# Optimization experiments

Hardware: AMD Instinct MI355X
Metric: run time of the kernel (lower is better)

## Reference

```python
import jax, jax.numpy as jnp
import numpy as np

N_NODES = 16384
N_GRAPHS = 64
NODES_PER_GRAPH = N_NODES // N_GRAPHS
F_IN = 128
E_DIM = 256
N_HEADS = 8
MLP = 1024
N_LAYERS = 4
N_CLASSES = 10
N_EDGES = 262144
LN_EPS = 1e-5


def setup_inputs() -> dict:
    key = jax.random.key(0)
    ks = jax.random.split(key, 32)
    s = 0.02
    inp = {
        "x": jax.random.normal(ks[0], (N_NODES, F_IN), jnp.float32),
        "edge_idx": jax.random.randint(ks[1], (2, N_EDGES), 0, N_NODES, jnp.int32),
        "batch": (jnp.arange(N_NODES, dtype=jnp.int32) // NODES_PER_GRAPH),
        "pos_enc": jax.random.normal(ks[2], (N_NODES, E_DIM), jnp.float32),
        # GCNConv params (torch Linear convention: W is [out, in])
        "gcn_w": jax.random.normal(ks[3], (F_IN, F_IN), jnp.float32) * s,
        "gcn_b": jnp.zeros((F_IN,), jnp.float32),
        "cls": jax.random.normal(ks[4], (E_DIM,), jnp.float32),
        "emb_w": jax.random.normal(ks[5], (E_DIM, F_IN), jnp.float32) * s,
        "emb_b": jnp.zeros((E_DIM,), jnp.float32),
        # stacked transformer-encoder-layer params over L layers
        "in_w": jax.random.normal(ks[6], (N_LAYERS, 3 * E_DIM, E_DIM), jnp.float32) * s,
        "in_b": jnp.zeros((N_LAYERS, 3 * E_DIM), jnp.float32),
        "out_w": jax.random.normal(ks[7], (N_LAYERS, E_DIM, E_DIM), jnp.float32) * s,
        "out_b": jnp.zeros((N_LAYERS, E_DIM), jnp.float32),
        "lin1_w": jax.random.normal(ks[8], (N_LAYERS, MLP, E_DIM), jnp.float32) * s,
        "lin1_b": jnp.zeros((N_LAYERS, MLP), jnp.float32),
        "lin2_w": jax.random.normal(ks[9], (N_LAYERS, E_DIM, MLP), jnp.float32) * s,
        "lin2_b": jnp.zeros((N_LAYERS, E_DIM), jnp.float32),
        "ln1_g": jnp.ones((N_LAYERS, E_DIM), jnp.float32),
        "ln1_beta": jnp.zeros((N_LAYERS, E_DIM), jnp.float32),
        "ln2_g": jnp.ones((N_LAYERS, E_DIM), jnp.float32),
        "ln2_beta": jnp.zeros((N_LAYERS, E_DIM), jnp.float32),
        "fc_w": jax.random.normal(ks[10], (N_CLASSES, E_DIM), jnp.float32) * s,
        "fc_b": jnp.zeros((N_CLASSES,), jnp.float32),
    }
    return inp


def _layer_norm(h, g, b):
    mu = jnp.mean(h, axis=-1, keepdims=True)
    var = jnp.mean(jnp.square(h - mu), axis=-1, keepdims=True)
    return (h - mu) * jax.lax.rsqrt(var + LN_EPS) * g + b


def _gcn_conv(x, edge_idx, gcn_w, gcn_b):
    # PyG GCNConv: lin -> add self-loops -> sym-normalized scatter-add -> +bias
    xw = x @ gcn_w.T                                             # [N, F]
    ar = jnp.arange(N_NODES, dtype=edge_idx.dtype)
    ei = jnp.concatenate([edge_idx, jnp.stack([ar, ar])], axis=1)
    row, col = ei[0], ei[1]
    deg = jax.ops.segment_sum(jnp.ones(ei.shape[1], xw.dtype), col, num_segments=N_NODES)
    dinv = jax.lax.rsqrt(deg)                                    # deg >= 1 (self loops)
    norm = dinv[row] * dinv[col]                                 # [E+N]
    out = jax.ops.segment_sum(norm[:, None] * xw[row], col, num_segments=N_NODES)
    return out + gcn_b


def reference(x, edge_idx, batch, pos_enc, gcn_w, gcn_b, cls, emb_w, emb_b,
              in_w, in_b, out_w, out_b, lin1_w, lin1_b, lin2_w, lin2_b,
              ln1_g, ln1_beta, ln2_g, ln2_beta, fc_w, fc_b):
    h = _gcn_conv(x, edge_idx, gcn_w, gcn_b)
    h = jax.nn.relu(h)
    h = h @ emb_w.T + emb_b + pos_enc                            # [N, E_DIM]
    # batch = arange // NODES_PER_GRAPH (contiguous equal-size graphs):
    # per-graph loop == batched reshape
    h = h.reshape(N_GRAPHS, NODES_PER_GRAPH, E_DIM)
    cls_tok = jnp.broadcast_to(cls, (N_GRAPHS, 1, E_DIM))
    h = jnp.concatenate([cls_tok, h], axis=1)                    # [G, S, E]
    S = NODES_PER_GRAPH + 1
    dh = E_DIM // N_HEADS
    scale = 1.0 / jnp.sqrt(jnp.asarray(dh, h.dtype))
    for l in range(N_LAYERS):
        # post-LN TransformerEncoderLayer (torch default), dropout off
        qkv = jnp.einsum('gse,fe->gsf', h, in_w[l]) + in_b[l]    # [G, S, 3E]
        q, k, v = jnp.split(qkv, 3, axis=-1)
        q = q.reshape(N_GRAPHS, S, N_HEADS, dh).transpose(0, 2, 1, 3)
        k = k.reshape(N_GRAPHS, S, N_HEADS, dh).transpose(0, 2, 1, 3)
        v = v.reshape(N_GRAPHS, S, N_HEADS, dh).transpose(0, 2, 1, 3)
        att = jax.nn.softmax(jnp.einsum('ghqd,ghkd->ghqk', q, k) * scale, axis=-1)
        o = jnp.einsum('ghqk,ghkd->ghqd', att, v)
        o = o.transpose(0, 2, 1, 3).reshape(N_GRAPHS, S, E_DIM)
        o = jnp.einsum('gse,fe->gsf', o, out_w[l]) + out_b[l]
        h = _layer_norm(h + o, ln1_g[l], ln1_beta[l])
        f = jax.nn.relu(jnp.einsum('gse,me->gsm', h, lin1_w[l]) + lin1_b[l])
        f = jnp.einsum('gsm,em->gse', f, lin2_w[l]) + lin2_b[l]
        h = _layer_norm(h + f, ln2_g[l], ln2_beta[l])
    cls_out = h[:, 0, :]                                         # [G, E]
    return cls_out @ fc_w.T + fc_b                               # [G, C]
```

## Files before the change

### kernel.cpp

```cpp
#include <hip/hip_runtime.h>
#include <cstddef>

#define N_NODES 16384
#define N_GRAPHS 64
#define NPG 256
#define F_IN 128
#define E_DIM 256
#define N_HEADS 8
#define DH 32
#define MLP 1024
#define N_LAYERS 4
#define N_CLASSES 10
#define N_EDGES 262144
#define S_LEN 257
#define M_ROWS (N_GRAPHS * S_LEN)
#define M_PAD 16512
#define LN_EPS 1e-5f

typedef __attribute__((ext_vector_type(8))) short bf16x8;
typedef __attribute__((ext_vector_type(4))) float f32x4;

__device__ inline unsigned short f2b1(float f) {
    unsigned u = __float_as_uint(f);
    unsigned r = (u + 0x7fffu + ((u >> 16) & 1u)) >> 16;
    return (unsigned short)r;
}

#define GLOBAL_LOAD_LDS16(g, l) \
    __builtin_amdgcn_global_load_lds((__attribute__((address_space(1))) const void*)(g), \
                                     (__attribute__((address_space(3))) void*)(l), 16, 0, 0)

__global__ void f2b4(const float* __restrict__ in, unsigned short* __restrict__ out, int n4) {
    int i = blockIdx.x * 256 + threadIdx.x;
    if (i < n4) {
        float4 v = ((const float4*)in)[i];
        ushort4 o;
        o.x = f2b1(v.x); o.y = f2b1(v.y); o.z = f2b1(v.z); o.w = f2b1(v.w);
        ((ushort4*)out)[i] = o;
    }
}

__global__ __launch_bounds__(256) void gemm_mfma(
    const unsigned short* __restrict__ A, const unsigned short* __restrict__ W,
    const float* __restrict__ bias, const float* __restrict__ add,
    float* __restrict__ outF, unsigned short* __restrict__ outB,
    int M, int N, int K, int relu)
{
    __shared__ __align__(16) unsigned short As[128 * 32];
    __shared__ __align__(16) unsigned short Bs[128 * 32];
    const int tid = threadIdx.x;
    const int wave = tid >> 6;
    const int lane = tid & 63;
    const int bm = blockIdx.y * 128;
    const int bn = blockIdx.x * 128;

    const int srow = (lane >> 2);
    const int scol = (lane & 3) * 8;
    const size_t a_r0 = (size_t)(bm + wave * 16 + srow) * K + scol;
    const size_t b_r0 = (size_t)(bn + wave * 16 + srow) * K + scol;
    unsigned short* ldsA0 = &As[wave * 512];
    unsigned short* ldsA1 = &As[(wave + 4) * 512];
    unsigned short* ldsB0 = &Bs[wave * 512];
    unsigned short* ldsB1 = &Bs[(wave + 4) * 512];

    const int wm = (wave & 1) * 64;
    const int wn = (wave >> 1) * 64;
    const int fr = lane & 15;
    const int fk = (lane >> 4) * 8;

    f32x4 acc[4][4];
#pragma unroll
    for (int i = 0; i < 4; ++i)
#pragma unroll
        for (int j = 0; j < 4; ++j)
            acc[i][j] = (f32x4){0.f, 0.f, 0.f, 0.f};

    for (int k0 = 0; k0 < K; k0 += 32) {
        __syncthreads();
        GLOBAL_LOAD_LDS16(A + a_r0 + k0, ldsA0);
        GLOBAL_LOAD_LDS16(A + a_r0 + (size_t)64 * K + k0, ldsA1);
        GLOBAL_LOAD_LDS16(W + b_r0 + k0, ldsB0);
        GLOBAL_LOAD_LDS16(W + b_r0 + (size_t)64 * K + k0, ldsB1);
        __syncthreads();

        bf16x8 a[4], b[4];
#pragma unroll
        for (int i = 0; i < 4; ++i)
            a[i] = *(const bf16x8*)&As[(wm + i * 16 + fr) * 32 + fk];
#pragma unroll
        for (int j = 0; j < 4; ++j)
            b[j] = *(const bf16x8*)&Bs[(wn + j * 16 + fr) * 32 + fk];
#pragma unroll
        for (int i = 0; i < 4; ++i)
#pragma unroll
            for (int j = 0; j < 4; ++j)
                acc[i][j] = __builtin_amdgcn_mfma_f32_16x16x32_bf16(a[i], b[j], acc[i][j], 0, 0, 0);
    }

    const int er = (lane >> 4) * 4;
    const int ec = lane & 15;
#pragma unroll
    for (int j = 0; j < 4; ++j) {
        const int col = bn + wn + j * 16 + ec;
        const float bs = bias ? bias[col] : 0.f;
#pragma unroll
        for (int i = 0; i < 4; ++i) {
#pragma unroll
            for (int r = 0; r < 4; ++r) {
                const int row = bm + wm + i * 16 + er + r;
                float v = acc[i][j][r] + bs;
                if (add)  v += add[(size_t)row * N + col];
                if (relu) v = fmaxf(v, 0.f);
                if (outF) outF[(size_t)row * N + col] = v;
                if (outB) outB[(size_t)row * N + col] = f2b1(v);
            }
        }
    }
}

__global__ void deg_count(const int* __restrict__ ei, float* __restrict__ deg) {
    int e = blockIdx.x * blockDim.x + threadIdx.x;
    if (e < N_EDGES) atomicAdd(&deg[ei[N_EDGES + e]], 1.0f);
}

__global__ void make_dinv(float* __restrict__ deg) {
    int i = blockIdx.x * blockDim.x + threadIdx.x;
    if (i < N_NODES) deg[i] = rsqrtf(deg[i] + 1.0f);
}

__global__ void edge_agg(const float* __restrict__ xw, const float* __restrict__ dinv,
                         const int* __restrict__ ei, float* __restrict__ agg) {
    int e = blockIdx.x;
    int f = threadIdx.x;
    int r = ei[e];
    int c = ei[N_EDGES + e];
    float nrm = dinv[r] * dinv[c];
    atomicAdd(&agg[(size_t)c * F_IN + f], nrm * xw[(size_t)r * F_IN + f]);
}

__global__ void gcn_finish(const float* __restrict__ agg, const float* __restrict__ xw,
                           const float* __restrict__ dinv, const float* __restrict__ b,
                           unsigned short* __restrict__ aggb) {
    int i = blockIdx.x;
    int f = threadIdx.x;
    float di = dinv[i];
    size_t idx = (size_t)i * F_IN + f;
    float v = agg[idx] + di * di * xw[idx] + b[f];
    aggb[idx] = f2b1(fmaxf(v, 0.f));
}

__global__ void assemble_h(const float* __restrict__ emb, const float* __restrict__ cls,
                           float* __restrict__ h, unsigned short* __restrict__ hb) {
    int row = blockIdx.x;
    int f = threadIdx.x;
    int g = row / S_LEN, s = row % S_LEN;
    float v = (s == 0) ? cls[f] : emb[((size_t)g * NPG + (s - 1)) * E_DIM + f];
    h[(size_t)row * E_DIM + f] = v;
    hb[(size_t)row * E_DIM + f] = f2b1(v);
}

__global__ __launch_bounds__(256) void attn_mfma(const unsigned short* __restrict__ qkvb,
                                                 unsigned short* __restrict__ ob) {
    const int g  = blockIdx.x >> 3;
    const int hh = blockIdx.x & 7;
    __shared__ __align__(16) unsigned short Ks[272 * 32];
    __shared__ __align__(16) unsigned short VT[32 * 288];
    __shared__ __align__(16) unsigned short Ps[4 * 16 * 288];
    const int tid  = threadIdx.x;
    const int wave = tid >> 6;
    const int lane = tid & 63;
    const int quad = lane >> 4;
    const int l16  = lane & 15;
    const size_t grow0 = (size_t)g * S_LEN;

    for (int s = tid; s < 272; s += 256) {
        uint4* dst = (uint4*)&Ks[s * 32];
        if (s < S_LEN) {
            const uint4* src = (const uint4*)(qkvb + (grow0 + s) * 768 + 256 + hh * 32);
            dst[0] = src[0]; dst[1] = src[1]; dst[2] = src[2]; dst[3] = src[3];
        } else {
            uint4 z = {0u, 0u, 0u, 0u};
            dst[0] = z; dst[1] = z; dst[2] = z; dst[3] = z;
        }
    }
    for (int s = tid; s < 288; s += 256) {
        unsigned short t[32];
        if (s < S_LEN) {
            const uint4* src = (const uint4*)(qkvb + (grow0 + s) * 768 + 512 + hh * 32);
            ((uint4*)t)[0] = src[0]; ((uint4*)t)[1] = src[1];
            ((uint4*)t)[2] = src[2]; ((uint4*)t)[3] = src[3];
        } else {
#pragma unroll
            for (int d = 0; d < 32; ++d) t[d] = 0;
        }
#pragma unroll
        for (int d = 0; d < 32; ++d) VT[d * 288 + s] = t[d];
    }
    unsigned short* Pw = &Ps[wave * 16 * 288];
    for (int i = lane; i < 256; i += 64)
        Pw[(i >> 4) * 288 + 272 + (i & 15)] = 0;
    __syncthreads();

    const float scale = 0.17677669529663687f;
    for (int qt = wave; qt < 17; qt += 4) {
        const int qrow_l = qt * 16 + l16;
        bf16x8 aq = *(const bf16x8*)(qkvb + (grow0 + qrow_l) * 768 + hh * 32 + quad * 8);

        f32x4 sc[17];
#pragma unroll
        for (int kt = 0; kt < 17; ++kt) {
            bf16x8 bk = *(const bf16x8*)&Ks[(kt * 16 + l16) * 32 + quad * 8];
            f32x4 z = (f32x4){0.f, 0.f, 0.f, 0.f};
            sc[kt] = __builtin_amdgcn_mfma_f32_16x16x32_bf16(aq, bk, z, 0, 0, 0);
        }

        float lsum[4] = {0.f, 0.f, 0.f, 0.f};
#pragma unroll
        for (int kt = 0; kt < 17; ++kt) {
#pragma unroll
            for (int r = 0; r < 4; ++r) {
                float p = __expf(sc[kt][r] * scale);
                if (kt == 16 && l16 != 0) p = 0.f;
                lsum[r] += p;
                Pw[(quad * 4 + r) * 288 + kt * 16 + l16] = f2b1(p);
            }
        }
#pragma unroll
        for (int r = 0; r < 4; ++r) {
            float s = lsum[r];
            s += __shfl_xor(s, 1, 64);
            s += __shfl_xor(s, 2, 64);
            s += __shfl_xor(s, 4, 64);
            s += __shfl_xor(s, 8, 64);
            lsum[r] = s;
        }

        f32x4 o0 = (f32x4){0.f, 0.f, 0.f, 0.f};
        f32x4 o1 = (f32x4){0.f, 0.f, 0.f, 0.f};
#pragma unroll
        for (int c = 0; c < 9; ++c) {
            bf16x8 ap  = *(const bf16x8*)&Pw[l16 * 288 + c * 32 + quad * 8];
            bf16x8 bv0 = *(const bf16x8*)&VT[l16 * 288 + c * 32 + quad * 8];
            bf16x8 bv1 = *(const bf16x8*)&VT[(16 + l16) * 288 + c * 32 + quad * 8];
            o0 = __builtin_amdgcn_mfma_f32_16x16x32_bf16(ap, bv0, o0, 0, 0, 0);
            o1 = __builtin_amdgcn_mfma_f32_16x16x32_bf16(ap, bv1, o1, 0, 0, 0);
        }

#pragma unroll
        for (int r = 0; r < 4; ++r) {
            int row_l = qt * 16 + quad * 4 + r;
            if (row_l < S_LEN) {
                float inv = 1.f / lsum[r];
                size_t orow = (grow0 + row_l) * E_DIM + hh * 32;
                ob[orow + l16]      = f2b1(o0[r] * inv);
                ob[orow + 16 + l16] = f2b1(o1[r] * inv);
            }
        }
    }
}

__global__ __launch_bounds__(256) void ln_residual(float* __restrict__ h, const float* __restrict__ res,
                                                   const float* __restrict__ g, const float* __restrict__ b,
                                                   unsigned short* __restrict__ hb) {
    __shared__ float ws1[4], ws2[4];
    __shared__ float mu_s, rstd_s;
    const int row = blockIdx.x;
    const int t = threadIdx.x;
    size_t idx = (size_t)row * E_DIM + t;
    float v = h[idx] + res[idx];
    float s1 = v, s2 = v * v;
#pragma unroll
    for (int off = 32; off > 0; off >>= 1) {
        s1 += __shfl_down(s1, off, 64);
        s2 += __shfl_down(s2, off, 64);
    }
    int wid = t >> 6, lane = t & 63;
    if (lane == 0) { ws1[wid] = s1; ws2[wid] = s2; }
    __syncthreads();
    if (t == 0) {
        float a1 = ws1[0] + ws1[1] + ws1[2] + ws1[3];
        float a2 = ws2[0] + ws2[1] + ws2[2] + ws2[3];
        float mu = a1 * (1.f / 256.f);
        float var = a2 * (1.f / 256.f) - mu * mu;
        mu_s = mu;
        rstd_s = rsqrtf(var + LN_EPS);
    }
    __syncthreads();
    float o = (v - mu_s) * rstd_s * g[t] + b[t];
    h[idx] = o;
    hb[idx] = f2b1(o);
}

__global__ void fc_kernel(const float* __restrict__ h, const float* __restrict__ w,
                          const float* __restrict__ b, float* __restrict__ out) {
    int g = blockIdx.x;
    __shared__ float row[E_DIM];
    int t = threadIdx.x;
    row[t] = h[(size_t)g * S_LEN * E_DIM + t];
    __syncthreads();
    if (t < N_CLASSES) {
        float s = 0.f;
        for (int j = 0; j < E_DIM; ++j) s += row[j] * w[t * E_DIM + j];
        out[g * N_CLASSES + t] = s + b[t];
    }
}

extern "C" void kernel_launch(void* const* d_in, const int* in_sizes, int n_in,
                              void* d_out, int out_size, void* d_ws, size_t ws_size,
                              hipStream_t stream) {
    const float* x       = (const float*)d_in[0];
    const int*   edgei   = (const int*)  d_in[1];
    const float* pos_enc = (const float*)d_in[3];
    const float* gcn_w   = (const float*)d_in[4];
    const float* gcn_b   = (const float*)d_in[5];
    const float* cls     = (const float*)d_in[6];
    const float* emb_w   = (const float*)d_in[7];
    const float* emb_b   = (const float*)d_in[8];
    const float* in_w    = (const float*)d_in[9];
    const float* in_b    = (const float*)d_in[10];
    const float* out_w   = (const float*)d_in[11];
    const float* out_b   = (const float*)d_in[12];
    const float* lin1_w  = (const float*)d_in[13];
    const float* lin1_b  = (const float*)d_in[14];
    const float* lin2_w  = (const float*)d_in[15];
    const float* lin2_b  = (const float*)d_in[16];
    const float* ln1_g   = (const float*)d_in[17];
    const float* ln1_be  = (const float*)d_in[18];
    const float* ln2_g   = (const float*)d_in[19];
    const float* ln2_be  = (const float*)d_in[20];
    const float* fc_w    = (const float*)d_in[21];
    const float* fc_b    = (const float*)d_in[22];
    float* out = (float*)d_out;

    float* ws = (float*)d_ws;
    float* h    = ws;
    float* tmp  = h    + (size_t)M_PAD * E_DIM;
    float* qkv  = tmp  + (size_t)M_PAD * E_DIM;
    float* xw   = qkv  + (size_t)M_PAD * 768;
    float* agg  = xw   + (size_t)N_NODES * F_IN;
    float* deg  = agg  + (size_t)N_NODES * F_IN;
    unsigned short* ub     = (unsigned short*)(deg + N_NODES);
    unsigned short* hb     = ub;
    unsigned short* attnob = hb     + (size_t)M_PAD * E_DIM;
    unsigned short* fbufb  = attnob + (size_t)M_PAD * E_DIM;
    unsigned short* xb     = fbufb  + (size_t)M_PAD * MLP;
    unsigned short* aggb   = xb     + (size_t)N_NODES * F_IN;
    unsigned short* gcn_wb = aggb   + (size_t)N_NODES * F_IN;
    unsigned short* emb_wb = gcn_wb + (size_t)F_IN * F_IN;
    unsigned short* in_wb  = emb_wb + (size_t)E_DIM * F_IN;
    unsigned short* out_wb = in_wb  + (size_t)N_LAYERS * 768 * E_DIM;
    unsigned short* lin1_wb= out_wb + (size_t)N_LAYERS * E_DIM * E_DIM;
    unsigned short* lin2_wb= lin1_wb+ (size_t)N_LAYERS * MLP * E_DIM;
    float* emb_out = qkv;
    unsigned short* qkvb = (unsigned short*)qkv;

    f2b4<<<(N_NODES * F_IN / 4 + 255) / 256, 256, 0, stream>>>(x, xb, N_NODES * F_IN / 4);
    f2b4<<<(F_IN * F_IN / 4 + 255) / 256, 256, 0, stream>>>(gcn_w, gcn_wb, F_IN * F_IN / 4);
    f2b4<<<(E_DIM * F_IN / 4 + 255) / 256, 256, 0, stream>>>(emb_w, emb_wb, E_DIM * F_IN / 4);
    f2b4<<<(N_LAYERS * 768 * E_DIM / 4 + 255) / 256, 256, 0, stream>>>(in_w, in_wb, N_LAYERS * 768 * E_DIM / 4);
    f2b4<<<(N_LAYERS * E_DIM * E_DIM / 4 + 255) / 256, 256, 0, stream>>>(out_w, out_wb, N_LAYERS * E_DIM * E_DIM / 4);
    f2b4<<<(N_LAYERS * MLP * E_DIM / 4 + 255) / 256, 256, 0, stream>>>(lin1_w, lin1_wb, N_LAYERS * MLP * E_DIM / 4);
    f2b4<<<(N_LAYERS * E_DIM * MLP / 4 + 255) / 256, 256, 0, stream>>>(lin2_w, lin2_wb, N_LAYERS * E_DIM * MLP / 4);

    hipMemsetAsync(deg, 0, N_NODES * sizeof(float), stream);
    hipMemsetAsync(agg, 0, (size_t)N_NODES * F_IN * sizeof(float), stream);
    deg_count<<<(N_EDGES + 255) / 256, 256, 0, stream>>>(edgei, deg);
    make_dinv<<<(N_NODES + 255) / 256, 256, 0, stream>>>(deg);
    gemm_mfma<<<dim3(F_IN / 128, N_NODES / 128), 256, 0, stream>>>(
        xb, gcn_wb, nullptr, nullptr, xw, nullptr, N_NODES, F_IN, F_IN, 0);
    edge_agg<<<N_EDGES, F_IN, 0, stream>>>(xw, deg, edgei, agg);
    gcn_finish<<<N_NODES, F_IN, 0, stream>>>(agg, xw, deg, gcn_b, aggb);

    gemm_mfma<<<dim3(E_DIM / 128, N_NODES / 128), 256, 0, stream>>>(
        aggb, emb_wb, emb_b, pos_enc, emb_out, nullptr, N_NODES, E_DIM, F_IN, 0);
    assemble_h<<<M_ROWS, E_DIM, 0, stream>>>(emb_out, cls, h, hb);

    for (int l = 0; l < N_LAYERS; ++l) {
        gemm_mfma<<<dim3(768 / 128, M_PAD / 128), 256, 0, stream>>>(
            hb, in_wb + (size_t)l * 768 * E_DIM, in_b + (size_t)l * 768, nullptr,
            nullptr, qkvb, M_PAD, 768, E_DIM, 0);
        attn_mfma<<<N_GRAPHS * N_HEADS, 256, 0, stream>>>(qkvb, attnob);
        gemm_mfma<<<dim3(E_DIM / 128, M_PAD / 128), 256, 0, stream>>>(
            attnob, out_wb + (size_t)l * E_DIM * E_DIM, out_b + (size_t)l * E_DIM, nullptr,
            tmp, nullptr, M_PAD, E_DIM, E_DIM, 0);
        ln_residual<<<M_ROWS, E_DIM, 0, stream>>>(h, tmp, ln1_g + l * E_DIM, ln1_be + l * E_DIM, hb);
        gemm_mfma<<<dim3(MLP / 128, M_PAD / 128), 256, 0, stream>>>(
            hb, lin1_wb + (size_t)l * MLP * E_DIM, lin1_b + (size_t)l * MLP, nullptr,
            nullptr, fbufb, M_PAD, MLP, E_DIM, 1);
        gemm_mfma<<<dim3(E_DIM / 128, M_PAD / 128), 256, 0, stream>>>(
            fbufb, lin2_wb + (size_t)l * E_DIM * MLP, lin2_b + (size_t)l * E_DIM, nullptr,
            tmp, nullptr, M_PAD, E_DIM, MLP, 0);
        ln_residual<<<M_ROWS, E_DIM, 0, stream>>>(h, tmp, ln2_g + l * E_DIM, ln2_be + l * E_DIM, hb);
    }

    fc_kernel<<<N_GRAPHS, E_DIM, 0, stream>>>(h, fc_w, fc_b, out);
}
```

Before: 944.7 us.

## Fuse LayerNorm into projection GEMMs, CSR-gather GCN aggregation, batch weight casts

Replaces the out-projection and MLP-down GEMMs plus separate residual LayerNorm kernels with a single full-row GEMM that applies bias, residual and LayerNorm in its epilogue, removing the fp32 temp round trip. GCN aggregation is rebuilt as a CSR layout (degree scan plus edge scatter) followed by a per-node gather, replacing per-feature float atomics. The seven bf16 cast launches are merged into one grid-stride kernel. Risks include lower GEMM parallelism in the 64-row fused tiles, a single-block scan, and nondeterministic edge order within CSR rows.

```diff
diff --git a/kernel.cpp b/kernel.cpp
--- a/kernel.cpp
+++ b/kernel.cpp
@@ -30,13 +30,23 @@
     __builtin_amdgcn_global_load_lds((__attribute__((address_space(1))) const void*)(g), \
                                      (__attribute__((address_space(3))) void*)(l), 16, 0, 0)
 
-__global__ void f2b4(const float* __restrict__ in, unsigned short* __restrict__ out, int n4) {
-    int i = blockIdx.x * 256 + threadIdx.x;
-    if (i < n4) {
-        float4 v = ((const float4*)in)[i];
-        ushort4 o;
-        o.x = f2b1(v.x); o.y = f2b1(v.y); o.z = f2b1(v.z); o.w = f2b1(v.w);
-        ((ushort4*)out)[i] = o;
+struct F2BJobs {
+    const float* src[7];
+    unsigned short* dst[7];
+    int n4[7];
+};
+__global__ __launch_bounds__(256) void f2b_all(F2BJobs jobs) {
+#pragma unroll 1
+    for (int r = 0; r < 7; ++r) {
+        const float4* s = (const float4*)jobs.src[r];
+        ushort4* d = (ushort4*)jobs.dst[r];
+        const int n4 = jobs.n4[r];
+        for (int i = blockIdx.x * 256 + threadIdx.x; i < n4; i += gridDim.x * 256) {
+            float4 v = s[i];
+            ushort4 o;
+            o.x = f2b1(v.x); o.y = f2b1(v.y); o.z = f2b1(v.z); o.w = f2b1(v.w);
+            d[i] = o;
+        }
     }
 }
 
@@ -118,35 +128,153 @@
     }
 }
 
+__global__ __launch_bounds__(256) void gemm_ln(
+    const unsigned short* __restrict__ A, const unsigned short* __restrict__ W,
+    const float* __restrict__ bias, const float* __restrict__ g,
+    const float* __restrict__ beta,
+    float* __restrict__ h, unsigned short* __restrict__ hb, int K)
+{
+    __shared__ __align__(16) unsigned short As[64 * 32];
+    __shared__ __align__(16) unsigned short Bs[256 * 32];
+    const int tid  = threadIdx.x;
+    const int wave = tid >> 6;
+    const int lane = tid & 63;
+    const int quad = lane >> 4;
+    const int l16  = lane & 15;
+    const int bm   = blockIdx.x * 64;
+
+    const int srow = lane >> 2;
+    const int scol = (lane & 3) * 8;
+    const size_t a_r0 = (size_t)(bm + wave * 16 + srow) * K + scol;
+    unsigned short* ldsA = &As[wave * 512];
+
+    f32x4 acc[16];
+#pragma unroll
+    for (int j = 0; j < 16; ++j) acc[j] = (f32x4){0.f, 0.f, 0.f, 0.f};
+
+    for (int k0 = 0; k0 < K; k0 += 32) {
+        __syncthreads();
+        GLOBAL_LOAD_LDS16(A + a_r0 + k0, ldsA);
+#pragma unroll
+        for (int cc = 0; cc < 4; ++cc) {
+            const int c = wave + cc * 4;
+            GLOBAL_LOAD_LDS16(W + (size_t)(c * 16 + srow) * K + scol + k0, &Bs[c * 512]);
+        }
+        __syncthreads();
+        bf16x8 a = *(const bf16x8*)&As[(wave * 16 + l16) * 32 + quad * 8];
+#pragma unroll
+        for (int j = 0; j < 16; ++j) {
+            bf16x8 b = *(const bf16x8*)&Bs[(j * 16 + l16) * 32 + quad * 8];
+            acc[j] = __builtin_amdgcn_mfma_f32_16x16x32_bf16(a, b, acc[j], 0, 0, 0);
+        }
+    }
+
+    const int row0 = bm + wave * 16 + quad * 4;
+    float gv[16], bv[16], biasv[16];
+#pragma unroll
+    for (int j = 0; j < 16; ++j) {
+        const int col = j * 16 + l16;
+        gv[j] = g[col]; bv[j] = beta[col]; biasv[j] = bias[col];
+    }
+#pragma unroll
+    for (int r = 0; r < 4; ++r) {
+        const int row = row0 + r;
+        float v[16];
+        float s1 = 0.f, s2 = 0.f;
+#pragma unroll
+        for (int j = 0; j < 16; ++j) {
+            const int col = j * 16 + l16;
+            float t = acc[j][r] + biasv[j] + h[(size_t)row * E_DIM + col];
+            v[j] = t; s1 += t; s2 += t * t;
+        }
+        s1 += __shfl_xor(s1, 1, 64); s2 += __shfl_xor(s2, 1, 64);
+        s1 += __shfl_xor(s1, 2, 64); s2 += __shfl_xor(s2, 2, 64);
+        s1 += __shfl_xor(s1, 4, 64); s2 += __shfl_xor(s2, 4, 64);
+        s1 += __shfl_xor(s1, 8, 64); s2 += __shfl_xor(s2, 8, 64);
+        const float mu = s1 * (1.f / 256.f);
+        const float var = s2 * (1.f / 256.f) - mu * mu;
+        const float rstd = rsqrtf(var + LN_EPS);
+#pragma unroll
+        for (int j = 0; j < 16; ++j) {
+            const int col = j * 16 + l16;
+            float o = (v[j] - mu) * rstd * gv[j] + bv[j];
+            h[(size_t)row * E_DIM + col] = o;
+            hb[(size_t)row * E_DIM + col] = f2b1(o);
+        }
+    }
+}
+
 __global__ void deg_count(const int* __restrict__ ei, float* __restrict__ deg) {
     int e = blockIdx.x * blockDim.x + threadIdx.x;
     if (e < N_EDGES) atomicAdd(&deg[ei[N_EDGES + e]], 1.0f);
 }
 
+__global__ __launch_bounds__(1024) void scan_deg(const float* __restrict__ deg,
+                                                 int* __restrict__ row_start) {
+    __shared__ int lds[1024];
+    const int t = threadIdx.x;
+    const int base = t * 16;
+    int loc[16];
+    int s = 0;
+#pragma unroll
+    for (int i = 0; i < 16; ++i) { loc[i] = s; s += (int)deg[base + i]; }
+    lds[t] = s;
+    __syncthreads();
+    for (int off = 1; off < 1024; off <<= 1) {
+        int v = lds[t];
+        int u = (t >= off) ? lds[t - off] : 0;
+        __syncthreads();
+        lds[t] = v + u;
+        __syncthreads();
+    }
+    const int excl = (t == 0) ? 0 : lds[t - 1];
+#pragma unroll
+    for (int i = 0; i < 16; ++i) row_start[base + i] = excl + loc[i];
+    if (t == 1023) row_start[16384] = lds[1023];
+}
+
 __global__ void make_dinv(float* __restrict__ deg) {
     int i = blockIdx.x * blockDim.x + threadIdx.x;
     if (i < N_NODES) deg[i] = rsqrtf(deg[i] + 1.0f);
 }
 
-__global__ void edge_agg(const float* __restrict__ xw, const float* __restrict__ dinv,
-                         const int* __restrict__ ei, float* __restrict__ agg) {
-    int e = blockIdx.x;
-    int f = threadIdx.x;
-    int r = ei[e];
-    int c = ei[N_EDGES + e];
-    float nrm = dinv[r] * dinv[c];
-    atomicAdd(&agg[(size_t)c * F_IN + f], nrm * xw[(size_t)r * F_IN + f]);
-}
-
-__global__ void gcn_finish(const float* __restrict__ agg, const float* __restrict__ xw,
-                           const float* __restrict__ dinv, const float* __restrict__ b,
-                           unsigned short* __restrict__ aggb) {
-    int i = blockIdx.x;
-    int f = threadIdx.x;
-    float di = dinv[i];
-    size_t idx = (size_t)i * F_IN + f;
-    float v = agg[idx] + di * di * xw[idx] + b[f];
-    aggb[idx] = f2b1(fmaxf(v, 0.f));
+__global__ void scatter_edges(const int* __restrict__ ei, const float* __restrict__ dinv,
+                              const int* __restrict__ row_start, int* __restrict__ cursor,
+                              int* __restrict__ esrc, float* __restrict__ enrm) {
+    int e = blockIdx.x * 256 + threadIdx.x;
+    if (e < N_EDGES) {
+        int r = ei[e], c = ei[N_EDGES + e];
+        int slot = atomicAdd(&cursor[c], 1);
+        int p = row_start[c] + slot;
+        esrc[p] = r;
+        enrm[p] = dinv[r] * dinv[c];
+    }
+}
+
+__global__ __launch_bounds__(256) void gcn_gather(
+    const float* __restrict__ xw, const int* __restrict__ row_start,
+    const int* __restrict__ esrc, const float* __restrict__ enrm,
+    const float* __restrict__ dinv, const float* __restrict__ bias,
+    unsigned short* __restrict__ aggb) {
+    const int n = blockIdx.x * 4 + (threadIdx.x >> 6);
+    const int t = threadIdx.x & 63;
+    const int e0 = row_start[n], e1 = row_start[n + 1];
+    float ax = 0.f, ay = 0.f;
+    for (int e = e0; e < e1; ++e) {
+        int s = esrc[e];
+        float w = enrm[e];
+        float2 v = ((const float2*)(xw + (size_t)s * F_IN))[t];
+        ax += w * v.x; ay += w * v.y;
+    }
+    const float di = dinv[n];
+    const float w0 = di * di;
+    float2 vs = ((const float2*)(xw + (size_t)n * F_IN))[t];
+    ax += w0 * vs.x; ay += w0 * vs.y;
+    float2 b2 = ((const float2*)bias)[t];
+    ushort2 o;
+    o.x = f2b1(fmaxf(ax + b2.x, 0.f));
+    o.y = f2b1(fmaxf(ay + b2.y, 0.f));
+    ((ushort2*)(aggb + (size_t)n * F_IN))[t] = o;
 }
 
 __global__ void assemble_h(const float* __restrict__ emb, const float* __restrict__ cls,
@@ -257,38 +385,6 @@
             }
         }
     }
-}
-
-__global__ __launch_bounds__(256) void ln_residual(float* __restrict__ h, const float* __restrict__ res,
-                                                   const float* __restrict__ g, const float* __restrict__ b,
-                                                   unsigned short* __restrict__ hb) {
-    __shared__ float ws1[4], ws2[4];
-    __shared__ float mu_s, rstd_s;
-    const int row = blockIdx.x;
-    const int t = threadIdx.x;
-    size_t idx = (size_t)row * E_DIM + t;
-    float v = h[idx] + res[idx];
-    float s1 = v, s2 = v * v;
-#pragma unroll
-    for (int off = 32; off > 0; off >>= 1) {
-        s1 += __shfl_down(s1, off, 64);
-        s2 += __shfl_down(s2, off, 64);
-    }
-    int wid = t >> 6, lane = t & 63;
-    if (lane == 0) { ws1[wid] = s1; ws2[wid] = s2; }
-    __syncthreads();
-    if (t == 0) {
-        float a1 = ws1[0] + ws1[1] + ws1[2] + ws1[3];
-        float a2 = ws2[0] + ws2[1] + ws2[2] + ws2[3];
-        float mu = a1 * (1.f / 256.f);
-        float var = a2 * (1.f / 256.f) - mu * mu;
-        mu_s = mu;
-        rstd_s = rsqrtf(var + LN_EPS);
-    }
-    __syncthreads();
-    float o = (v - mu_s) * rstd_s * g[t] + b[t];
-    h[idx] = o;
-    hb[idx] = f2b1(o);
 }
 
 __global__ void fc_kernel(const float* __restrict__ h, const float* __restrict__ w,
@@ -334,12 +430,14 @@
 
     float* ws = (float*)d_ws;
     float* h    = ws;
-    float* tmp  = h    + (size_t)M_PAD * E_DIM;
-    float* qkv  = tmp  + (size_t)M_PAD * E_DIM;
-    float* xw   = qkv  + (size_t)M_PAD * 768;
-    float* agg  = xw   + (size_t)N_NODES * F_IN;
-    float* deg  = agg  + (size_t)N_NODES * F_IN;
-    unsigned short* ub     = (unsigned short*)(deg + N_NODES);
+    float* qkv  = h   + (size_t)M_PAD * E_DIM;
+    float* xw   = qkv + (size_t)M_PAD * 768;
+    float* deg  = xw  + (size_t)N_NODES * F_IN;
+    int*   cursor    = (int*)(deg + N_NODES);
+    int*   row_start = cursor + N_NODES;
+    int*   esrc      = row_start + N_NODES + 1;
+    float* enrm      = (float*)(esrc + N_EDGES);
+    unsigned short* ub     = (unsigned short*)(enrm + N_EDGES);
     unsigned short* hb     = ub;
     unsigned short* attnob = hb     + (size_t)M_PAD * E_DIM;
     unsigned short* fbufb  = attnob + (size_t)M_PAD * E_DIM;
@@ -354,22 +452,24 @@
     float* emb_out = qkv;
     unsigned short* qkvb = (unsigned short*)qkv;
 
-    f2b4<<<(N_NODES * F_IN / 4 + 255) / 256, 256, 0, stream>>>(x, xb, N_NODES * F_IN / 4);
-    f2b4<<<(F_IN * F_IN / 4 + 255) / 256, 256, 0, stream>>>(gcn_w, gcn_wb, F_IN * F_IN / 4);
-    f2b4<<<(E_DIM * F_IN / 4 + 255) / 256, 256, 0, stream>>>(emb_w, emb_wb, E_DIM * F_IN / 4);
-    f2b4<<<(N_LAYERS * 768 * E_DIM / 4 + 255) / 256, 256, 0, stream>>>(in_w, in_wb, N_LAYERS * 768 * E_DIM / 4);
-    f2b4<<<(N_LAYERS * E_DIM * E_DIM / 4 + 255) / 256, 256, 0, stream>>>(out_w, out_wb, N_LAYERS * E_DIM * E_DIM / 4);
-    f2b4<<<(N_LAYERS * MLP * E_DIM / 4 + 255) / 256, 256, 0, stream>>>(lin1_w, lin1_wb, N_LAYERS * MLP * E_DIM / 4);
-    f2b4<<<(N_LAYERS * E_DIM * MLP / 4 + 255) / 256, 256, 0, stream>>>(lin2_w, lin2_wb, N_LAYERS * E_DIM * MLP / 4);
-
-    hipMemsetAsync(deg, 0, N_NODES * sizeof(float), stream);
-    hipMemsetAsync(agg, 0, (size_t)N_NODES * F_IN * sizeof(float), stream);
+    F2BJobs jobs;
+    jobs.src[0] = x;      jobs.dst[0] = xb;      jobs.n4[0] = N_NODES * F_IN / 4;
+    jobs.src[1] = gcn_w;  jobs.dst[1] = gcn_wb;  jobs.n4[1] = F_IN * F_IN / 4;
+    jobs.src[2] = emb_w;  jobs.dst[2] = emb_wb;  jobs.n4[2] = E_DIM * F_IN / 4;
+    jobs.src[3] = in_w;   jobs.dst[3] = in_wb;   jobs.n4[3] = N_LAYERS * 768 * E_DIM / 4;
+    jobs.src[4] = out_w;  jobs.dst[4] = out_wb;  jobs.n4[4] = N_LAYERS * E_DIM * E_DIM / 4;
+    jobs.src[5] = lin1_w; jobs.dst[5] = lin1_wb; jobs.n4[5] = N_LAYERS * MLP * E_DIM / 4;
+    jobs.src[6] = lin2_w; jobs.dst[6] = lin2_wb; jobs.n4[6] = N_LAYERS * E_DIM * MLP / 4;
+    f2b_all<<<1024, 256, 0, stream>>>(jobs);
+
+    hipMemsetAsync(deg, 0, 2 * N_NODES * sizeof(float), stream);
     deg_count<<<(N_EDGES + 255) / 256, 256, 0, stream>>>(edgei, deg);
+    scan_deg<<<1, 1024, 0, stream>>>(deg, row_start);
     make_dinv<<<(N_NODES + 255) / 256, 256, 0, stream>>>(deg);
     gemm_mfma<<<dim3(F_IN / 128, N_NODES / 128), 256, 0, stream>>>(
         xb, gcn_wb, nullptr, nullptr, xw, nullptr, N_NODES, F_IN, F_IN, 0);
-    edge_agg<<<N_EDGES, F_IN, 0, stream>>>(xw, deg, edgei, agg);
-    gcn_finish<<<N_NODES, F_IN, 0, stream>>>(agg, xw, deg, gcn_b, aggb);
+    scatter_edges<<<(N_EDGES + 255) / 256, 256, 0, stream>>>(edgei, deg, row_start, cursor, esrc, enrm);
+    gcn_gather<<<N_NODES / 4, 256, 0, stream>>>(xw, row_start, esrc, enrm, deg, gcn_b, aggb);
 
     gemm_mfma<<<dim3(E_DIM / 128, N_NODES / 128), 256, 0, stream>>>(
         aggb, emb_wb, emb_b, pos_enc, emb_out, nullptr, N_NODES, E_DIM, F_IN, 0);
@@ -380,17 +480,15 @@
             hb, in_wb + (size_t)l * 768 * E_DIM, in_b + (size_t)l * 768, nullptr,
             nullptr, qkvb, M_PAD, 768, E_DIM, 0);
         attn_mfma<<<N_GRAPHS * N_HEADS, 256, 0, stream>>>(qkvb, attnob);
-        gemm_mfma<<<dim3(E_DIM / 128, M_PAD / 128), 256, 0, stream>>>(
-            attnob, out_wb + (size_t)l * E_DIM * E_DIM, out_b + (size_t)l * E_DIM, nullptr,
-            tmp, nullptr, M_PAD, E_DIM, E_DIM, 0);
-        ln_residual<<<M_ROWS, E_DIM, 0, stream>>>(h, tmp, ln1_g + l * E_DIM, ln1_be + l * E_DIM, hb);
+        gemm_ln<<<M_PAD / 64, 256, 0, stream>>>(
+            attnob, out_wb + (size_t)l * E_DIM * E_DIM, out_b + (size_t)l * E_DIM,
+            ln1_g + l * E_DIM, ln1_be + l * E_DIM, h, hb, E_DIM);
         gemm_mfma<<<dim3(MLP / 128, M_PAD / 128), 256, 0, stream>>>(
             hb, lin1_wb + (size_t)l * MLP * E_DIM, lin1_b + (size_t)l * MLP, nullptr,
             nullptr, fbufb, M_PAD, MLP, E_DIM, 1);
-        gemm_mfma<<<dim3(E_DIM / 128, M_PAD / 128), 256, 0, stream>>>(
-            fbufb, lin2_wb + (size_t)l * E_DIM * MLP, lin2_b + (size_t)l * E_DIM, nullptr,
-            tmp, nullptr, M_PAD, E_DIM, MLP, 0);
-        ln_residual<<<M_ROWS, E_DIM, 0, stream>>>(h, tmp, ln2_g + l * E_DIM, ln2_be + l * E_DIM, hb);
+        gemm_ln<<<M_PAD / 64, 256, 0, stream>>>(
+            fbufb, lin2_wb + (size_t)l * E_DIM * MLP, lin2_b + (size_t)l * E_DIM,
+            ln2_g + l * E_DIM, ln2_be + l * E_DIM, h, hb, MLP);
     }
 
     fc_kernel<<<N_GRAPHS, E_DIM, 0, stream>>>(h, fc_w, fc_b, out);
```

Result: faster. 889.9 us (-5.8%).
